# Kernel tuning notes

Hardware: AMD Instinct MI355X
Metric: run time of the kernel (lower is better)

Reference implementation:

```python
import jax, jax.numpy as jnp
import numpy as np

N, D, C, TOPK = 4096, 512, 512, 5


def setup_inputs() -> dict:
    key = jax.random.key(0)
    k1, k2, k3, k4 = jax.random.split(key, 4)
    feat1 = jax.random.normal(k1, (N, D), dtype=jnp.float32)
    feat2 = jax.random.normal(k2, (N, D), dtype=jnp.float32)
    # probs are softmax outputs in the original pipeline -> valid BCE inputs in (0,1)
    prob1 = jax.nn.softmax(jax.random.normal(k3, (N, C), dtype=jnp.float32), axis=-1)
    prob2 = jax.nn.softmax(jax.random.normal(k4, (N, C), dtype=jnp.float32), axis=-1)
    return {"feat1": feat1, "feat2": feat2, "prob1": prob1, "prob2": prob2, "topk": TOPK}


def reference(feat1, feat2, prob1, prob2, topk):
    # rank statistics on detached feat1: top-k feature indices, sorted as a set
    rank_idx = jnp.argsort(-feat1, axis=1)           # descending argsort, (N, D)
    top = jnp.sort(rank_idx[:, :topk], axis=1)       # (N, K) sorted top-k index sets
    # pair_enum layout: pair k = j*N + i with x1 -> row i (fast), x2 -> row j (slow).
    # Build the equivalent (N, N) matrices with rows=j, cols=i.
    rank_diff = jnp.abs(top[None, :, :] - top[:, None, :]).sum(-1)  # (N, N)
    target = (rank_diff == 0).astype(prob1.dtype)
    # pred_sim[k] = dot(prob1[i], prob2[j])  ->  P[j, i]
    pred_sim = prob2 @ prob1.T                        # (N, N)
    # BCELoss with torch's log clamp at -100
    log_p = jnp.clip(jnp.log(pred_sim), -100.0)
    log_1mp = jnp.clip(jnp.log(1.0 - pred_sim), -100.0)
    loss = -jnp.mean(target * log_p + (1.0 - target) * log_1mp)
    return loss
```

## Files before the change

### kernel.cpp

```cpp
#include <hip/hip_runtime.h>
#include <hip/hip_bf16.h>
#include <stdint.h>

#define NROWS 4096
#define CDIM  512
#define TOPK  5
#define BM    128
#define BK    32

typedef __bf16 bf16x8 __attribute__((ext_vector_type(8)));
typedef float  f32x4  __attribute__((ext_vector_type(4)));

__global__ void convert_kernel(const float* __restrict__ p1,
                               const float* __restrict__ p2,
                               __bf16* __restrict__ o1,
                               __bf16* __restrict__ o2) {
  const int t = blockIdx.x * 256 + threadIdx.x;
  const float* src;
  __bf16* dst;
  int e = t;
  if (t >= 262144) { src = p2; dst = o2; e = t - 262144; }
  else             { src = p1; dst = o1; }
  const int row   = e >> 6;
  const int k8    = e & 63;
  const int chunk = k8 >> 2;
  const int slot  = k8 & 3;
  const int dslot = slot ^ ((row >> 1) & 3);
  const float4 a = *(const float4*)(src + (size_t)row * CDIM + k8 * 8);
  const float4 b = *(const float4*)(src + (size_t)row * CDIM + k8 * 8 + 4);
  bf16x8 v;
  v[0]=(__bf16)a.x; v[1]=(__bf16)a.y; v[2]=(__bf16)a.z; v[3]=(__bf16)a.w;
  v[4]=(__bf16)b.x; v[5]=(__bf16)b.y; v[6]=(__bf16)b.z; v[7]=(__bf16)b.w;
  *(bf16x8*)(dst + (size_t)row * CDIM + chunk * 32 + dslot * 8) = v;
}

__global__ void topk_keys_kernel(const float* __restrict__ feat1,
                                 unsigned long long* __restrict__ keys) {
  const int row = blockIdx.x;
  const int l   = threadIdx.x;
  const float* r = feat1 + (size_t)row * CDIM;
  float v[8];
  const float4 a = *(const float4*)(r + l * 8);
  const float4 b = *(const float4*)(r + l * 8 + 4);
  v[0]=a.x; v[1]=a.y; v[2]=a.z; v[3]=a.w;
  v[4]=b.x; v[5]=b.y; v[6]=b.z; v[7]=b.w;

  int sel[TOPK];
#pragma unroll
  for (int s = 0; s < TOPK; ++s) {
    float bv = -__builtin_inff();
    int   bi = 0x7fffffff;
#pragma unroll
    for (int t = 0; t < 8; ++t) {
      if (v[t] > bv) { bv = v[t]; bi = l * 8 + t; }
    }
#pragma unroll
    for (int off = 32; off > 0; off >>= 1) {
      float ov = __shfl_xor(bv, off);
      int   oi = __shfl_xor(bi, off);
      if (ov > bv || (ov == bv && oi < bi)) { bv = ov; bi = oi; }
    }
    sel[s] = bi;
    const int loc = bi - l * 8;
    if (loc >= 0 && loc < 8) v[loc] = -__builtin_inff();
  }

#define CSWAP(x, y) { int mn = min(sel[x], sel[y]); int mx = max(sel[x], sel[y]); sel[x] = mn; sel[y] = mx; }
  CSWAP(0,1) CSWAP(3,4) CSWAP(2,4) CSWAP(2,3) CSWAP(1,4)
  CSWAP(0,3) CSWAP(0,2) CSWAP(1,3) CSWAP(1,2)
#undef CSWAP

  if (l == 0) {
    unsigned long long key =
        (unsigned long long)sel[0]
      | ((unsigned long long)sel[1] << 9)
      | ((unsigned long long)sel[2] << 18)
      | ((unsigned long long)sel[3] << 27)
      | ((unsigned long long)sel[4] << 36);
    keys[row] = key;
  }
}

__global__ __launch_bounds__(256) void
gemm_loss_kernel(const __bf16* __restrict__ p1b,
                 const __bf16* __restrict__ p2b,
                 const unsigned long long* __restrict__ keys,
                 float* __restrict__ partials) {
  __shared__ __bf16 sm[2][2 * BM * BK];
  __shared__ float  red[256];

  const int tid = threadIdx.x;
  const int bi = blockIdx.x, bj = blockIdx.y;
  const int ib = bi * BM, jb = bj * BM;

  const int l  = tid & 63, w = tid >> 6;
  const int wr = w >> 1,  wc = w & 1;
  const int lr = l & 15,  kq = l >> 4;

  f32x4 acc[4][4] = {};

  auto stage = [&](int buf, int k0) {
#pragma unroll
    for (int i = 0; i < 2; ++i) {
      const int c    = (w * 2 + i) * 64 + l;
      const int row  = c >> 2;
      const int slot = c & 3;
      const __bf16* gA = p2b + (size_t)(jb + row) * CDIM + k0 + slot * 8;
      const __bf16* gB = p1b + (size_t)(ib + row) * CDIM + k0 + slot * 8;
      __bf16* lA = &sm[buf][(w * 2 + i) * 512];
      __bf16* lB = &sm[buf][BM * BK + (w * 2 + i) * 512];
      __builtin_amdgcn_global_load_lds(
          (const __attribute__((address_space(1))) unsigned int*)(const void*)gA,
          (__attribute__((address_space(3))) unsigned int*)(void*)lA, 16, 0, 0);
      __builtin_amdgcn_global_load_lds(
          (const __attribute__((address_space(1))) unsigned int*)(const void*)gB,
          (__attribute__((address_space(3))) unsigned int*)(void*)lB, 16, 0, 0);
    }
  };

  stage(0, 0);
  __syncthreads();

  int cur = 0;
  for (int k0 = 0; k0 < CDIM; k0 += BK) {
    if (k0 + BK < CDIM) stage(cur ^ 1, k0 + BK);

    bf16x8 af[4], bfr[4];
#pragma unroll
    for (int m = 0; m < 4; ++m) {
      const int arow = wr * 64 + m * 16 + lr;
      const int ps   = kq ^ ((arow >> 1) & 3);
      af[m] = *(const bf16x8*)&sm[cur][arow * BK + ps * 8];
    }
#pragma unroll
    for (int n = 0; n < 4; ++n) {
      const int brow = wc * 64 + n * 16 + lr;
      const int ps   = kq ^ ((brow >> 1) & 3);
      bfr[n] = *(const bf16x8*)&sm[cur][BM * BK + brow * BK + ps * 8];
    }
#pragma unroll
    for (int m = 0; m < 4; ++m)
#pragma unroll
      for (int n = 0; n < 4; ++n)
        acc[m][n] = __builtin_amdgcn_mfma_f32_16x16x32_bf16(af[m], bfr[n], acc[m][n], 0, 0, 0);

    __syncthreads();
    cur ^= 1;
  }

  unsigned long long kj[16], ki[4];
#pragma unroll
  for (int m = 0; m < 4; ++m)
#pragma unroll
    for (int r = 0; r < 4; ++r)
      kj[m * 4 + r] = keys[jb + wr * 64 + m * 16 + kq * 4 + r];
#pragma unroll
  for (int n = 0; n < 4; ++n)
    ki[n] = keys[ib + wc * 64 + n * 16 + lr];

  float sum = 0.f;
#pragma unroll
  for (int m = 0; m < 4; ++m)
#pragma unroll
    for (int n = 0; n < 4; ++n)
#pragma unroll
      for (int r = 0; r < 4; ++r) {
        const float p = acc[m][n][r];
        const bool  t = (kj[m * 4 + r] == ki[n]);
        const float x = t ? p : (1.0f - p);
        sum += fmaxf(__logf(x), -100.0f);
      }

  red[tid] = sum;
  __syncthreads();
  for (int s = 128; s > 0; s >>= 1) {
    if (tid < s) red[tid] += red[tid + s];
    __syncthreads();
  }
  if (tid == 0) partials[blockIdx.y * gridDim.x + blockIdx.x] = red[0];
}

__global__ void finalize_kernel(const float* __restrict__ partials,
                                float* __restrict__ out) {
  __shared__ float red[256];
  float s = 0.f;
  for (int i = threadIdx.x; i < 1024; i += 256) s += partials[i];
  red[threadIdx.x] = s;
  __syncthreads();
  for (int st = 128; st > 0; st >>= 1) {
    if (threadIdx.x < st) red[threadIdx.x] += red[threadIdx.x + st];
    __syncthreads();
  }
  if (threadIdx.x == 0) out[0] = -red[0] * (1.0f / 16777216.0f);
}

extern "C" void kernel_launch(void* const* d_in, const int* in_sizes, int n_in,
                              void* d_out, int out_size, void* d_ws, size_t ws_size,
                              hipStream_t stream) {
  (void)in_sizes; (void)n_in; (void)out_size; (void)ws_size;
  const float* feat1 = (const float*)d_in[0];
  const float* prob1 = (const float*)d_in[2];
  const float* prob2 = (const float*)d_in[3];

  __bf16* o1 = (__bf16*)d_ws;
  __bf16* o2 = (__bf16*)((char*)d_ws + (size_t)NROWS * CDIM * 2);
  unsigned long long* keys = (unsigned long long*)((char*)d_ws + (size_t)NROWS * CDIM * 4);
  float* partials = (float*)((char*)d_ws + (size_t)NROWS * CDIM * 4 + NROWS * 8);

  convert_kernel<<<2048, 256, 0, stream>>>(prob1, prob2, o1, o2);
  topk_keys_kernel<<<NROWS, 64, 0, stream>>>(feat1, keys);
  gemm_loss_kernel<<<dim3(32, 32), 256, 0, stream>>>(o1, o2, keys, partials);
  finalize_kernel<<<1, 256, 0, stream>>>(partials, (float*)d_out);
}
```

Before: 50.05 us.

## Use 256x256 tiles with 4-stage LDS pipeline and XCD-aware block mapping

Grows the GEMM tile to 256x256 with 512 threads and 8 waves, and replaces the double buffer with a 4-slot LDS ring that issues loads two tiles ahead, using explicit vmcnt waits and raw barriers. Block IDs are remapped so neighbouring tiles land on the same XCD for L2 reuse, and the LDS swizzle is changed to row&3 in both the convert and load paths. MFMA sections get raised wave priority. The bigger tiles cut global and LDS traffic per output, but the grid drops to 256 blocks, which may underfill 256 CUs, and register pressure rises with 128 accumulators per thread.

New measurement: 45.37 us. 1.1x faster.

```diff
diff --git a/kernel.cpp b/kernel.cpp
--- a/kernel.cpp
+++ b/kernel.cpp
@@ -5,8 +5,9 @@
 #define NROWS 4096
 #define CDIM  512
 #define TOPK  5
-#define BM    128
+#define BM    256
 #define BK    32
+#define NKT   16
 
 typedef __bf16 bf16x8 __attribute__((ext_vector_type(8)));
 typedef float  f32x4  __attribute__((ext_vector_type(4)));
@@ -25,7 +26,7 @@
   const int k8    = e & 63;
   const int chunk = k8 >> 2;
   const int slot  = k8 & 3;
-  const int dslot = slot ^ ((row >> 1) & 3);
+  const int dslot = slot ^ (row & 3);
   const float4 a = *(const float4*)(src + (size_t)row * CDIM + k8 * 8);
   const float4 b = *(const float4*)(src + (size_t)row * CDIM + k8 * 8 + 4);
   bf16x8 v;
@@ -81,34 +82,38 @@
   }
 }
 
-__global__ __launch_bounds__(256) void
+__global__ __launch_bounds__(512, 2) void
 gemm_loss_kernel(const __bf16* __restrict__ p1b,
                  const __bf16* __restrict__ p2b,
                  const unsigned long long* __restrict__ keys,
                  float* __restrict__ partials) {
-  __shared__ __bf16 sm[2][2 * BM * BK];
-  __shared__ float  red[256];
+  __shared__ __bf16 sm[4][2][BM * BK];
+  __shared__ float  red[512];
 
   const int tid = threadIdx.x;
-  const int bi = blockIdx.x, bj = blockIdx.y;
-  const int ib = bi * BM, jb = bj * BM;
-
-  const int l  = tid & 63, w = tid >> 6;
-  const int wr = w >> 1,  wc = w & 1;
-  const int lr = l & 15,  kq = l >> 4;
-
-  f32x4 acc[4][4] = {};
-
-  auto stage = [&](int buf, int k0) {
+  const int l   = tid & 63, w = tid >> 6;
+  const int wr  = w >> 2,  wc = w & 3;
+  const int lr  = l & 15,  kq = l >> 4;
+
+  const int bid = blockIdx.x;
+  const int x   = bid & 7, wv = bid >> 3;
+  const int it  = (x & 3) * 4 + (wv & 3);
+  const int jt  = (x >> 2) * 8 + (wv >> 2);
+  const int ib  = it * BM, jb = jt * BM;
+
+  f32x4 acc[8][4] = {};
+
+  auto stage = [&](int slot, int kt) {
+    const int k0 = kt * BK;
 #pragma unroll
     for (int i = 0; i < 2; ++i) {
-      const int c    = (w * 2 + i) * 64 + l;
-      const int row  = c >> 2;
-      const int slot = c & 3;
-      const __bf16* gA = p2b + (size_t)(jb + row) * CDIM + k0 + slot * 8;
-      const __bf16* gB = p1b + (size_t)(ib + row) * CDIM + k0 + slot * 8;
-      __bf16* lA = &sm[buf][(w * 2 + i) * 512];
-      __bf16* lB = &sm[buf][BM * BK + (w * 2 + i) * 512];
+      const int c   = i * 512 + tid;
+      const int row = c >> 2;
+      const int ps  = c & 3;
+      const __bf16* gA = p2b + (size_t)(jb + row) * CDIM + k0 + ps * 8;
+      const __bf16* gB = p1b + (size_t)(ib + row) * CDIM + k0 + ps * 8;
+      __bf16* lA = &sm[slot][0][(i * 512 + w * 64) * 8];
+      __bf16* lB = &sm[slot][1][(i * 512 + w * 64) * 8];
       __builtin_amdgcn_global_load_lds(
           (const __attribute__((address_space(1))) unsigned int*)(const void*)gA,
           (__attribute__((address_space(3))) unsigned int*)(void*)lA, 16, 0, 0);
@@ -118,74 +123,85 @@
     }
   };
 
-  stage(0, 0);
-  __syncthreads();
-
-  int cur = 0;
-  for (int k0 = 0; k0 < CDIM; k0 += BK) {
-    if (k0 + BK < CDIM) stage(cur ^ 1, k0 + BK);
-
-    bf16x8 af[4], bfr[4];
-#pragma unroll
-    for (int m = 0; m < 4; ++m) {
-      const int arow = wr * 64 + m * 16 + lr;
-      const int ps   = kq ^ ((arow >> 1) & 3);
-      af[m] = *(const bf16x8*)&sm[cur][arow * BK + ps * 8];
-    }
+  auto compute = [&](int slot) {
+    bf16x8 af[8], bfr[4];
 #pragma unroll
     for (int n = 0; n < 4; ++n) {
-      const int brow = wc * 64 + n * 16 + lr;
-      const int ps   = kq ^ ((brow >> 1) & 3);
-      bfr[n] = *(const bf16x8*)&sm[cur][BM * BK + brow * BK + ps * 8];
-    }
-#pragma unroll
-    for (int m = 0; m < 4; ++m)
+      const int r  = wc * 64 + n * 16 + lr;
+      const int ps = kq ^ (r & 3);
+      bfr[n] = *(const bf16x8*)&sm[slot][1][r * 32 + ps * 8];
+    }
+#pragma unroll
+    for (int m = 0; m < 8; ++m) {
+      const int r  = wr * 128 + m * 16 + lr;
+      const int ps = kq ^ (r & 3);
+      af[m] = *(const bf16x8*)&sm[slot][0][r * 32 + ps * 8];
+    }
+    __builtin_amdgcn_s_setprio(1);
+#pragma unroll
+    for (int m = 0; m < 8; ++m)
 #pragma unroll
       for (int n = 0; n < 4; ++n)
         acc[m][n] = __builtin_amdgcn_mfma_f32_16x16x32_bf16(af[m], bfr[n], acc[m][n], 0, 0, 0);
-
-    __syncthreads();
-    cur ^= 1;
-  }
-
-  unsigned long long kj[16], ki[4];
-#pragma unroll
-  for (int m = 0; m < 4; ++m)
+    __builtin_amdgcn_s_setprio(0);
+  };
+
+  stage(0, 0);
+  stage(1, 1);
+
+  for (int kt = 0; kt < NKT - 2; ++kt) {
+    stage((kt + 2) & 3, kt + 2);
+    asm volatile("s_waitcnt vmcnt(8)" ::: "memory");
+    __builtin_amdgcn_s_barrier();
+    __builtin_amdgcn_sched_barrier(0);
+    compute(kt & 3);
+  }
+  asm volatile("s_waitcnt vmcnt(4)" ::: "memory");
+  __builtin_amdgcn_s_barrier();
+  __builtin_amdgcn_sched_barrier(0);
+  compute((NKT - 2) & 3);
+  asm volatile("s_waitcnt vmcnt(0)" ::: "memory");
+  __builtin_amdgcn_s_barrier();
+  __builtin_amdgcn_sched_barrier(0);
+  compute((NKT - 1) & 3);
+
+  unsigned long long kj[32], ki[4];
+#pragma unroll
+  for (int m = 0; m < 8; ++m)
 #pragma unroll
     for (int r = 0; r < 4; ++r)
-      kj[m * 4 + r] = keys[jb + wr * 64 + m * 16 + kq * 4 + r];
+      kj[m * 4 + r] = keys[jb + wr * 128 + m * 16 + kq * 4 + r];
 #pragma unroll
   for (int n = 0; n < 4; ++n)
     ki[n] = keys[ib + wc * 64 + n * 16 + lr];
 
   float sum = 0.f;
 #pragma unroll
-  for (int m = 0; m < 4; ++m)
+  for (int m = 0; m < 8; ++m)
 #pragma unroll
     for (int n = 0; n < 4; ++n)
 #pragma unroll
       for (int r = 0; r < 4; ++r) {
         const float p = acc[m][n][r];
         const bool  t = (kj[m * 4 + r] == ki[n]);
-        const float x = t ? p : (1.0f - p);
-        sum += fmaxf(__logf(x), -100.0f);
+        const float xx = t ? p : (1.0f - p);
+        sum += fmaxf(__logf(xx), -100.0f);
       }
 
   red[tid] = sum;
   __syncthreads();
-  for (int s = 128; s > 0; s >>= 1) {
+#pragma unroll
+  for (int s = 256; s > 0; s >>= 1) {
     if (tid < s) red[tid] += red[tid + s];
     __syncthreads();
   }
-  if (tid == 0) partials[blockIdx.y * gridDim.x + blockIdx.x] = red[0];
+  if (tid == 0) partials[bid] = red[0];
 }
 
 __global__ void finalize_kernel(const float* __restrict__ partials,
                                 float* __restrict__ out) {
   __shared__ float red[256];
-  float s = 0.f;
-  for (int i = threadIdx.x; i < 1024; i += 256) s += partials[i];
-  red[threadIdx.x] = s;
+  red[threadIdx.x] = partials[threadIdx.x];
   __syncthreads();
   for (int st = 128; st > 0; st >>= 1) {
     if (threadIdx.x < st) red[threadIdx.x] += red[threadIdx.x + st];
@@ -209,6 +225,6 @@
 
   convert_kernel<<<2048, 256, 0, stream>>>(prob1, prob2, o1, o2);
   topk_keys_kernel<<<NROWS, 64, 0, stream>>>(feat1, keys);
-  gemm_loss_kernel<<<dim3(32, 32), 256, 0, stream>>>(o1, o2, keys, partials);
+  gemm_loss_kernel<<<256, 512, 0, stream>>>(o1, o2, keys, partials);
   finalize_kernel<<<1, 256, 0, stream>>>(partials, (float*)d_out);
 }
```
